# Performance work log

Measured on AMD Instinct MI355X. Metric: run time of the kernel, lower is better.

Reference implementation:

```python
import jax, jax.numpy as jnp
import numpy as np

M = 41
RHO = 4.0
HDIM = 10
NMODES = 2
BATCH = 16384


def triplet_index(m_size, rho):
    # reduced PBC triplet index set: n >= m, |m|,|n|,|m+n| <= (M-1)/2, |m*n| <= rho*(M-1)/2
    h = (m_size - 1) // 2
    idx = [(m, n) for m in range(-h, h + 1) for n in range(m, h + 1)
           if abs(m + n) <= h and abs(m * n) <= rho * h]
    return np.array(idx, dtype=np.int32)

IDX = triplet_index(M, RHO)
S = len(IDX)


def _c(a):
    # last-dim-2 real tensor -> complex
    return jax.lax.complex(a[..., 0], a[..., 1])


def setup_inputs() -> dict:
    key = jax.random.key(0)
    ks = jax.random.split(key, 6)
    x = jax.random.normal(ks[0], (BATCH, M, NMODES, 2), dtype=jnp.float32)
    task_info = jax.random.uniform(ks[1], (BATCH, 4), dtype=jnp.float32)  # col 0 = power in dBm
    pbc_C = 0.01 * jax.random.normal(ks[2], (S, 2), dtype=jnp.float32)  # complex PBC coeffs
    W1 = jax.random.normal(ks[3], (HDIM, NMODES, S, 2), dtype=jnp.float32) / np.sqrt(2.0 * NMODES * S)
    b1 = jnp.zeros((HDIM, 2), dtype=jnp.float32)
    W2 = jax.random.normal(ks[4], (HDIM, NMODES, M, 2), dtype=jnp.float32) / np.sqrt(2.0 * NMODES * M)
    b2 = jnp.zeros((HDIM, 2), dtype=jnp.float32)
    m_idx = jnp.asarray(IDX[:, 0], dtype=jnp.int32)
    n_idx = jnp.asarray(IDX[:, 1], dtype=jnp.int32)
    return {"x": x, "task_info": task_info, "pbc_C": pbc_C,
            "W1": W1, "b1": b1, "W2": W2, "b2": b2,
            "m_idx": m_idx, "n_idx": n_idx}


def _nonlinear_features(E, m_idx, n_idx):
    # E: [B, M, 2] complex -> [B, 2, S]; Manakov dual-pol triplets:
    # F[p] = (E[c+m,p]*conj(E[c+m+n,p]) + E[c+m,q]*conj(E[c+m+n,q])) * E[c+n,p]
    c = E.shape[1] // 2
    A = E[:, c + m_idx, :] * jnp.conj(E[:, c + m_idx + n_idx, :])  # [B, S, 2]
    F = (A + A[..., ::-1]) * E[:, c + n_idx, :]                    # [B, S, 2]
    return jnp.transpose(F, (0, 2, 1))                             # [B, 2, S]


def _conv_full(Wc, bc, inp):
    # ComplexConv1d whose kernel spans the whole input length (output length 1) -> [B, out]
    return jnp.einsum('oik,bik->bo', Wc, inp) + bc


def _forward(x, task_info, pbc_C, W1, b1, W2, b2, m_idx, n_idx):
    E = _c(x)                                    # [B, M, 2] complex64
    c = M // 2
    P = 10.0 ** (task_info[:, 0] / 10.0) / NMODES  # [B] launch power per mode
    F = _nonlinear_features(E, m_idx, n_idx)     # [B, 2, S]
    # EqAMPBC: center symbol + P * (triplet features . complex coeffs)
    pbc_out = E[:, c, :] + P[:, None] * jnp.einsum('bps,s->bp', F, _c(pbc_C))  # [B, 2]
    w1, bb1, w2, bb2 = _c(W1), _c(b1), _c(W2), _c(b2)
    # A = cat([f1(fo), f1(fo with pols flipped)], dim=-1) -> [B, hdim, 2]
    A = jnp.stack([_conv_full(w1, bb1, F), _conv_full(w1, bb1, F[:, ::-1, :])], axis=-1)
    Et = jnp.transpose(E, (0, 2, 1))             # [B, 2, M]
    Bm = jnp.stack([_conv_full(w2, bb2, Et), _conv_full(w2, bb2, Et[:, ::-1, :])], axis=-1)
    term = jnp.sum(A * Bm * jnp.conj(Bm) + jnp.conj(A) * Bm * Bm, axis=1)  # [B, 2]
    out = pbc_out + (1e-4 / np.sqrt(HDIM)) * term * (P[:, None] ** 2)
    return jnp.stack([out.real, out.imag], axis=-1)  # [B, 2, 2] float32


def reference(x, task_info, pbc_C, W1, b1, W2, b2, m_idx, n_idx):
    return _forward(x, task_info, pbc_C, W1, b1, W2, b2, m_idx, n_idx)
```

## Files before the change

kernel.cpp:

```cpp
#include <hip/hip_runtime.h>
#include <hip/hip_bf16.h>

typedef short bf16x8 __attribute__((ext_vector_type(8)));
typedef float f32x16 __attribute__((ext_vector_type(16)));

#define NCOL  32
#define KS1   112
#define KS2   12
#define ESTR  264

#define WP_OFF   0
#define W2P_OFF  344064

#define MET_OFF  10824
#define SUM_OFF  14544
#define LDS_BYTES 39120

__device__ __forceinline__ unsigned short f2bf(float f) {
    union { float f; unsigned u; } v; v.f = f;
    unsigned r = v.u + 0x7FFFu + ((v.u >> 16) & 1u);
    return (unsigned short)(r >> 16);
}
__device__ __forceinline__ float bfl(unsigned u) {
    union { unsigned q; float f; } v; v.q = u << 16; return v.f;
}
__device__ __forceinline__ float bfh(unsigned u) {
    union { unsigned q; float f; } v; v.q = u & 0xffff0000u; return v.f;
}
__device__ __forceinline__ unsigned pk2(float a, float b) {
    __hip_bfloat162 h = __float22bfloat162_rn(make_float2(a, b));
    unsigned u; __builtin_memcpy(&u, &h, 4); return u;
}
__device__ __forceinline__ bf16x8 asbf(uint4 v) {
    union { uint4 u; bf16x8 b; } z; z.u = v; return z.b;
}
__device__ __forceinline__ f32x16 zero16() {
    f32x16 z;
#pragma unroll
    for (int i = 0; i < 16; ++i) z[i] = 0.f;
    return z;
}

__global__ void prep_kernel(const float* __restrict__ W1,
                            const float* __restrict__ W2,
                            const float* __restrict__ pbcC,
                            unsigned short* __restrict__ Wp,
                            unsigned short* __restrict__ W2p, int S) {
    int idx = blockIdx.x * 256 + threadIdx.x;
    const int N1 = KS1 * 3 * 64 * 2;
    const int N2 = KS2 * 3 * 64 * 2;
    if (idx < N1) {
        int ks = idx / 384, rem = idx - ks * 384;
        int mt = rem >> 7; rem &= 127;
        int lane = rem >> 1, jh = rem & 1;
        int row = mt * 32 + (lane & 31);
        int kg  = ks * 16 + (lane >> 5) * 8 + jh * 4;
        int s   = kg >> 2;
        float2 wj0 = make_float2(0.f, 0.f), wj1 = make_float2(0.f, 0.f);
        int p = 0, r = 0;
        if (s < S) {
            if (row < 80) {
                int o = row >> 2; p = (row >> 1) & 1; r = row & 1;
                wj0 = ((const float2*)W1)[(size_t)(o * 2 + 0) * S + s];
                wj1 = ((const float2*)W1)[(size_t)(o * 2 + 1) * S + s];
            } else if (row < 84) {
                p = (row >> 1) & 1; r = row & 1;
                wj0 = ((const float2*)pbcC)[s];
            }
        }
        ushort4 h; unsigned short us[4];
#pragma unroll
        for (int t = 0; t < 4; ++t) {
            int i = t & 1, cc = t >> 1, j2 = i ^ p;
            float2 w = j2 ? wj1 : wj0;
            float v = (cc == 0) ? (r ? w.y : w.x) : (r ? w.x : -w.y);
            us[t] = f2bf(v);
        }
        h.x = us[0]; h.y = us[1]; h.z = us[2]; h.w = us[3];
        ((ushort4*)Wp)[idx] = h;
        return;
    }
    idx -= N1;
    if (idx < N2) {
        int ks = idx / 384, rem = idx - ks * 384;
        int mt = rem >> 7; rem &= 127;
        int lane = rem >> 1, jh = rem & 1;
        int row = mt * 32 + (lane & 31);
        int kg  = ks * 16 + (lane >> 5) * 8 + jh * 4;
        int m   = kg >> 2;
        float2 wj0 = make_float2(0.f, 0.f), wj1 = make_float2(0.f, 0.f);
        int p = 0, r = 0;
        if (m < 41 && row < 80) {
            int o = row >> 2; p = (row >> 1) & 1; r = row & 1;
            wj0 = ((const float2*)W2)[(o * 2 + 0) * 41 + m];
            wj1 = ((const float2*)W2)[(o * 2 + 1) * 41 + m];
        }
        ushort4 h; unsigned short us[4];
#pragma unroll
        for (int t = 0; t < 4; ++t) {
            int i = t & 1, cc = t >> 1, j2 = i ^ p;
            float2 w = j2 ? wj1 : wj0;
            float v = (cc == 0) ? (r ? w.y : w.x) : (r ? w.x : -w.y);
            us[t] = f2bf(v);
        }
        h.x = us[0]; h.y = us[1]; h.z = us[2]; h.w = us[3];
        ((ushort4*)W2p)[idx] = h;
    }
}

__global__ __launch_bounds__(256, 3) void eqsonn_kernel(
    const float* __restrict__ x, const float* __restrict__ task,
    const unsigned short* __restrict__ Wp,
    const unsigned short* __restrict__ W2p,
    const int* __restrict__ m_idx, const int* __restrict__ n_idx,
    const float* __restrict__ b1, const float* __restrict__ b2,
    float* __restrict__ out, int B, int S)
{
    __shared__ alignas(16) char ldsb[LDS_BYTES];
    const int tid  = threadIdx.x;
    const int lane = tid & 63;
    const int w    = __builtin_amdgcn_readfirstlane(tid >> 6);
    const int col  = lane & 31;
    const int kha  = lane >> 5;
    const int b0   = blockIdx.x * NCOL;

    for (int e = tid; e < 41 * NCOL; e += 256) {
        int bb = e / 41, k = e - bb * 41;
        int bs = b0 + bb; if (bs > B - 1) bs = B - 1;
        float4 v = ((const float4*)x)[(size_t)bs * 41 + k];
        ushort4 h;
        h.x = f2bf(v.x); h.y = f2bf(v.y); h.z = f2bf(v.z); h.w = f2bf(v.w);
        *(ushort4*)(ldsb + k * ESTR + bb * 8) = h;
    }
    for (int i = tid; i < 464; i += 256) {
        int m = 0, n = 0;
        if (i < S) { m = m_idx[i]; n = n_idx[i]; }
        unsigned offM = (unsigned)((20 + m) * ESTR);
        unsigned offB = (unsigned)((20 + m + n) * ESTR);
        unsigned offN = (unsigned)((20 + n) * ESTR);
        *(uint2*)(ldsb + MET_OFF + i * 8) = make_uint2(offM | (offB << 16), offN);
    }
    __syncthreads();

    const char* Ebase = ldsb + col * 8;
    auto ldM4 = [&](int ks) -> uint4 {
        return *(const uint4*)(ldsb + MET_OFF + (ks * 4 + kha * 2) * 8);
    };
    auto ldE = [&](unsigned off) -> uint2 {
        return *(const uint2*)(Ebase + off);
    };
    auto fbuild = [&](uint2 em, uint2 eq, uint2 en, unsigned& lo, unsigned& hi) {
        float m0r = bfl(em.x), m0i = bfh(em.x), m1r = bfl(em.y), m1i = bfh(em.y);
        float q0r = bfl(eq.x), q0i = bfh(eq.x), q1r = bfl(eq.y), q1i = bfh(eq.y);
        float n0r = bfl(en.x), n0i = bfh(en.x), n1r = bfl(en.y), n1i = bfh(en.y);
        float sr = m0r * q0r + m0i * q0i + m1r * q1r + m1i * q1i;
        float si = m0i * q0r - m0r * q0i + m1i * q1r - m1r * q1i;
        float F0r = sr * n0r - si * n0i, F0i = sr * n0i + si * n0r;
        float F1r = sr * n1r - si * n1i, F1i = sr * n1i + si * n1r;
        lo = pk2(F0r, F1r); hi = pk2(F0i, F1i);
    };

    f32x16 ac0 = zero16(), ac1 = zero16(), ac2 = zero16();
    {
        const int ks0 = w * 28;
        uint4 M = ldM4(ks0);
        uint2 e0 = ldE(M.x & 0xffffu), e1 = ldE(M.x >> 16), e2 = ldE(M.y);
        uint2 e3 = ldE(M.z & 0xffffu), e4 = ldE(M.z >> 16), e5 = ldE(M.w);
        uint4 Mc = ldM4(ks0 + 1);
        const short* Wp16 = (const short*)Wp;
        for (int ks = ks0; ks < ks0 + 28; ++ks) {
            const short* ap = Wp16 + (size_t)ks * 1536 + lane * 8;
            bf16x8 A0 = *(const bf16x8*)(ap);
            bf16x8 A1 = *(const bf16x8*)(ap + 512);
            bf16x8 A2 = *(const bf16x8*)(ap + 1024);
            uint2 f0 = ldE(Mc.x & 0xffffu), f1v = ldE(Mc.x >> 16), f2v = ldE(Mc.y);
            uint2 f3 = ldE(Mc.z & 0xffffu), f4v = ldE(Mc.z >> 16), f5v = ldE(Mc.w);
            uint4 Mn = ldM4(ks + 2);
            unsigned g0, g1, g2, g3;
            fbuild(e0, e1, e2, g0, g1);
            fbuild(e3, e4, e5, g2, g3);
            bf16x8 bfr = asbf(make_uint4(g0, g1, g2, g3));
            ac0 = __builtin_amdgcn_mfma_f32_32x32x16_bf16(A0, bfr, ac0, 0, 0, 0);
            ac1 = __builtin_amdgcn_mfma_f32_32x32x16_bf16(A1, bfr, ac1, 0, 0, 0);
            ac2 = __builtin_amdgcn_mfma_f32_32x32x16_bf16(A2, bfr, ac2, 0, 0, 0);
            e0 = f0; e1 = f1v; e2 = f2v; e3 = f3; e4 = f4v; e5 = f5v; Mc = Mn;
        }
    }

    __syncthreads();
    float* Sum = (float*)(ldsb + SUM_OFF);
    auto dump = [&](f32x16 a, int baserow, bool add) {
#pragma unroll
        for (int reg = 0; reg < 16; ++reg) {
            int row = baserow + (reg & 3) + 8 * (reg >> 2) + 4 * kha;
            int idx = row * 32 + col;
            if (add) Sum[idx] += a[reg]; else Sum[idx] = a[reg];
        }
    };
    for (int ph = 0; ph < 4; ++ph) {
        if (w == ph) {
            bool add = (ph != 0);
            dump(ac0, 0, add); dump(ac1, 32, add); dump(ac2, 64, add);
        }
        __syncthreads();
    }

    f32x16 bc0 = zero16(), bc1 = zero16(), bc2 = zero16();
    {
        const short* W216 = (const short*)W2p;
        for (int t = 0; t < 3; ++t) {
            int ks2 = w * 3 + t;
            const short* ap = W216 + (size_t)ks2 * 1536 + lane * 8;
            bf16x8 A0 = *(const bf16x8*)(ap);
            bf16x8 A1 = *(const bf16x8*)(ap + 512);
            bf16x8 A2 = *(const bf16x8*)(ap + 1024);
            unsigned g[4];
#pragma unroll
            for (int j = 0; j < 2; ++j) {
                int m = ks2 * 4 + kha * 2 + j;
                int mc = m < 41 ? m : 40;
                uint2 ue = *(const uint2*)(ldsb + mc * ESTR + col * 8);
                unsigned lo = (ue.x & 0xffffu) | (ue.y << 16);
                unsigned hi = (ue.x >> 16) | (ue.y & 0xffff0000u);
                if (m >= 41) { lo = 0u; hi = 0u; }
                g[j * 2] = lo; g[j * 2 + 1] = hi;
            }
            bf16x8 bfr = asbf(make_uint4(g[0], g[1], g[2], g[3]));
            bc0 = __builtin_amdgcn_mfma_f32_32x32x16_bf16(A0, bfr, bc0, 0, 0, 0);
            bc1 = __builtin_amdgcn_mfma_f32_32x32x16_bf16(A1, bfr, bc1, 0, 0, 0);
            bc2 = __builtin_amdgcn_mfma_f32_32x32x16_bf16(A2, bfr, bc2, 0, 0, 0);
        }
    }
    __syncthreads();
    for (int ph = 0; ph < 4; ++ph) {
        if (w == ph) {
            bool add = (ph != 0);
            dump(bc0, 96, add); dump(bc1, 128, add); dump(bc2, 160, add);
        }
        __syncthreads();
    }

    if (w == 0 && lane < NCOL) {
        int c = lane;
        float pr0 = Sum[80 * 32 + c], pi0 = Sum[81 * 32 + c];
        float pr1 = Sum[82 * 32 + c], pi1 = Sum[83 * 32 + c];
        float t0 = 0.f, t1 = 0.f, t2 = 0.f, t3 = 0.f;
#pragma unroll
        for (int o = 0; o < 10; ++o) {
            float b2r = b2[o * 2], b2i = b2[o * 2 + 1];
            float b1r = b1[o * 2], b1i = b1[o * 2 + 1];
            int rb = o * 4;
            float B0r = Sum[(96 + rb + 0) * 32 + c] + b2r;
            float B0i = Sum[(96 + rb + 1) * 32 + c] + b2i;
            float B1r = Sum[(96 + rb + 2) * 32 + c] + b2r;
            float B1i = Sum[(96 + rb + 3) * 32 + c] + b2i;
            float A0r = Sum[(rb + 0) * 32 + c] + b1r;
            float A0i = Sum[(rb + 1) * 32 + c] + b1i;
            float A1r = Sum[(rb + 2) * 32 + c] + b1r;
            float A1i = Sum[(rb + 3) * 32 + c] + b1i;
            float g0 = 2.f * (A0r * B0r + A0i * B0i);
            t0 += g0 * B0r; t1 += g0 * B0i;
            float g1 = 2.f * (A1r * B1r + A1i * B1i);
            t2 += g1 * B1r; t3 += g1 * B1i;
        }
        int b = b0 + c;
        if (b < B) {
            float dbm = task[(size_t)b * 4];
            float P   = exp2f(dbm * 0.33219280948873623f) * 0.5f;
            float kP2 = 3.1622776601683794e-05f * P * P;
            float4 Ec = ((const float4*)x)[(size_t)b * 41 + 20];
            float4 o4;
            o4.x = Ec.x + P * pr0 + kP2 * t0;
            o4.y = Ec.y + P * pi0 + kP2 * t1;
            o4.z = Ec.z + P * pr1 + kP2 * t2;
            o4.w = Ec.w + P * pi1 + kP2 * t3;
            ((float4*)out)[b] = o4;
        }
    }
}

extern "C" void kernel_launch(void* const* d_in, const int* in_sizes, int n_in,
                              void* d_out, int out_size, void* d_ws, size_t ws_size,
                              hipStream_t stream) {
    const float* x     = (const float*)d_in[0];
    const float* task  = (const float*)d_in[1];
    const float* pbcC  = (const float*)d_in[2];
    const float* W1    = (const float*)d_in[3];
    const float* b1    = (const float*)d_in[4];
    const float* W2    = (const float*)d_in[5];
    const float* b2    = (const float*)d_in[6];
    const int*   m_idx = (const int*)d_in[7];
    const int*   n_idx = (const int*)d_in[8];
    float* out = (float*)d_out;

    int S = in_sizes[7];
    int B = in_sizes[0] / (41 * 2 * 2);

    char* ws = (char*)d_ws;
    unsigned short* Wp  = (unsigned short*)(ws + WP_OFF);
    unsigned short* W2p = (unsigned short*)(ws + W2P_OFF);

    int prep_n = KS1 * 3 * 64 * 2 + KS2 * 3 * 64 * 2;
    prep_kernel<<<(prep_n + 255) / 256, 256, 0, stream>>>(W1, W2, pbcC, Wp, W2p, S);

    int grid = (B + NCOL - 1) / NCOL;
    eqsonn_kernel<<<grid, 256, 0, stream>>>(x, task, Wp, W2p, m_idx, n_idx,
                                            b1, b2, out, B, S);
}
```

Baseline: 101.7 us.

## Split K reduction across eight waves with dual LDS partial buffers and weight prefetch

Doubles the block to 512 threads so eight waves each handle 14 K-steps of the first GEMM instead of four waves handling 28. The waves reduce in two groups into two separate LDS sum buffers, which are then added together. The next step's weight fragments are also software-prefetched to hide global load latency. The cost is more LDS per block, an extra reduction pass and barriers, and a possible drop in occupancy because of the larger LDS footprint and register limits.

Result: faster. 98.08 us (-3.6%).

```diff
diff --git a/kernel.cpp b/kernel.cpp
--- a/kernel.cpp
+++ b/kernel.cpp
@@ -14,7 +14,8 @@
 
 #define MET_OFF  10824
 #define SUM_OFF  14544
-#define LDS_BYTES 39120
+#define SUM2_OFF 39120
+#define LDS_BYTES 63696
 
 __device__ __forceinline__ unsigned short f2bf(float f) {
     union { float f; unsigned u; } v; v.f = f;
@@ -108,7 +109,7 @@
     }
 }
 
-__global__ __launch_bounds__(256, 3) void eqsonn_kernel(
+__global__ __launch_bounds__(512, 4) void eqsonn_kernel(
     const float* __restrict__ x, const float* __restrict__ task,
     const unsigned short* __restrict__ Wp,
     const unsigned short* __restrict__ W2p,
@@ -124,7 +125,7 @@
     const int kha  = lane >> 5;
     const int b0   = blockIdx.x * NCOL;
 
-    for (int e = tid; e < 41 * NCOL; e += 256) {
+    for (int e = tid; e < 41 * NCOL; e += 512) {
         int bb = e / 41, k = e - bb * 41;
         int bs = b0 + bb; if (bs > B - 1) bs = B - 1;
         float4 v = ((const float4*)x)[(size_t)bs * 41 + k];
@@ -132,13 +133,13 @@
         h.x = f2bf(v.x); h.y = f2bf(v.y); h.z = f2bf(v.z); h.w = f2bf(v.w);
         *(ushort4*)(ldsb + k * ESTR + bb * 8) = h;
     }
-    for (int i = tid; i < 464; i += 256) {
+    if (tid < 464) {
         int m = 0, n = 0;
-        if (i < S) { m = m_idx[i]; n = n_idx[i]; }
+        if (tid < S) { m = m_idx[tid]; n = n_idx[tid]; }
         unsigned offM = (unsigned)((20 + m) * ESTR);
         unsigned offB = (unsigned)((20 + m + n) * ESTR);
         unsigned offN = (unsigned)((20 + n) * ESTR);
-        *(uint2*)(ldsb + MET_OFF + i * 8) = make_uint2(offM | (offB << 16), offN);
+        *(uint2*)(ldsb + MET_OFF + tid * 8) = make_uint2(offM | (offB << 16), offN);
     }
     __syncthreads();
 
@@ -162,17 +163,22 @@
 
     f32x16 ac0 = zero16(), ac1 = zero16(), ac2 = zero16();
     {
-        const int ks0 = w * 28;
+        const int ks0 = w * 14;
+        const short* Wp16 = (const short*)Wp;
         uint4 M = ldM4(ks0);
         uint2 e0 = ldE(M.x & 0xffffu), e1 = ldE(M.x >> 16), e2 = ldE(M.y);
         uint2 e3 = ldE(M.z & 0xffffu), e4 = ldE(M.z >> 16), e5 = ldE(M.w);
         uint4 Mc = ldM4(ks0 + 1);
-        const short* Wp16 = (const short*)Wp;
-        for (int ks = ks0; ks < ks0 + 28; ++ks) {
-            const short* ap = Wp16 + (size_t)ks * 1536 + lane * 8;
-            bf16x8 A0 = *(const bf16x8*)(ap);
-            bf16x8 A1 = *(const bf16x8*)(ap + 512);
-            bf16x8 A2 = *(const bf16x8*)(ap + 1024);
+        const short* ap0 = Wp16 + (size_t)ks0 * 1536 + lane * 8;
+        bf16x8 A0 = *(const bf16x8*)(ap0);
+        bf16x8 A1 = *(const bf16x8*)(ap0 + 512);
+        bf16x8 A2 = *(const bf16x8*)(ap0 + 1024);
+        for (int ks = ks0; ks < ks0 + 14; ++ks) {
+            int ksn = (ks + 1 < KS1) ? ks + 1 : KS1 - 1;
+            const short* apn = Wp16 + (size_t)ksn * 1536 + lane * 8;
+            bf16x8 N0 = *(const bf16x8*)(apn);
+            bf16x8 N1 = *(const bf16x8*)(apn + 512);
+            bf16x8 N2 = *(const bf16x8*)(apn + 1024);
             uint2 f0 = ldE(Mc.x & 0xffffu), f1v = ldE(Mc.x >> 16), f2v = ldE(Mc.y);
             uint2 f3 = ldE(Mc.z & 0xffffu), f4v = ldE(Mc.z >> 16), f5v = ldE(Mc.w);
             uint4 Mn = ldM4(ks + 2);
@@ -184,22 +190,24 @@
             ac1 = __builtin_amdgcn_mfma_f32_32x32x16_bf16(A1, bfr, ac1, 0, 0, 0);
             ac2 = __builtin_amdgcn_mfma_f32_32x32x16_bf16(A2, bfr, ac2, 0, 0, 0);
             e0 = f0; e1 = f1v; e2 = f2v; e3 = f3; e4 = f4v; e5 = f5v; Mc = Mn;
+            A0 = N0; A1 = N1; A2 = N2;
         }
     }
 
     __syncthreads();
-    float* Sum = (float*)(ldsb + SUM_OFF);
+    float* Reg = (float*)(ldsb + ((w < 4) ? SUM_OFF : SUM2_OFF));
+    const int ph = w & 3;
     auto dump = [&](f32x16 a, int baserow, bool add) {
 #pragma unroll
         for (int reg = 0; reg < 16; ++reg) {
             int row = baserow + (reg & 3) + 8 * (reg >> 2) + 4 * kha;
             int idx = row * 32 + col;
-            if (add) Sum[idx] += a[reg]; else Sum[idx] = a[reg];
+            if (add) Reg[idx] += a[reg]; else Reg[idx] = a[reg];
         }
     };
-    for (int ph = 0; ph < 4; ++ph) {
-        if (w == ph) {
-            bool add = (ph != 0);
+    for (int p = 0; p < 4; ++p) {
+        if (ph == p) {
+            bool add = (p != 0);
             dump(ac0, 0, add); dump(ac1, 32, add); dump(ac2, 64, add);
         }
         __syncthreads();
@@ -208,8 +216,7 @@
     f32x16 bc0 = zero16(), bc1 = zero16(), bc2 = zero16();
     {
         const short* W216 = (const short*)W2p;
-        for (int t = 0; t < 3; ++t) {
-            int ks2 = w * 3 + t;
+        for (int ks2 = w; ks2 < KS2; ks2 += 8) {
             const short* ap = W216 + (size_t)ks2 * 1536 + lane * 8;
             bf16x8 A0 = *(const bf16x8*)(ap);
             bf16x8 A1 = *(const bf16x8*)(ap + 512);
@@ -232,15 +239,29 @@
         }
     }
     __syncthreads();
-    for (int ph = 0; ph < 4; ++ph) {
-        if (w == ph) {
-            bool add = (ph != 0);
+    for (int p = 0; p < 4; ++p) {
+        if (ph == p) {
+            bool add = (p != 0);
             dump(bc0, 96, add); dump(bc1, 128, add); dump(bc2, 160, add);
         }
         __syncthreads();
     }
 
+    {
+        float4* S1 = (float4*)(ldsb + SUM_OFF);
+        float4* S2 = (float4*)(ldsb + SUM2_OFF);
+#pragma unroll
+        for (int i = 0; i < 3; ++i) {
+            int idx = tid + i * 512;
+            float4 a = S1[idx], b = S2[idx];
+            a.x += b.x; a.y += b.y; a.z += b.z; a.w += b.w;
+            S1[idx] = a;
+        }
+    }
+    __syncthreads();
+
     if (w == 0 && lane < NCOL) {
+        const float* Sum = (const float*)(ldsb + SUM_OFF);
         int c = lane;
         float pr0 = Sum[80 * 32 + c], pi0 = Sum[81 * 32 + c];
         float pr1 = Sum[82 * 32 + c], pi1 = Sum[83 * 32 + c];
@@ -304,6 +325,6 @@
     prep_kernel<<<(prep_n + 255) / 256, 256, 0, stream>>>(W1, W2, pbcC, Wp, W2p, S);
 
     int grid = (B + NCOL - 1) / NCOL;
-    eqsonn_kernel<<<grid, 256, 0, stream>>>(x, task, Wp, W2p, m_idx, n_idx,
+    eqsonn_kernel<<<grid, 512, 0, stream>>>(x, task, Wp, W2p, m_idx, n_idx,
                                             b1, b2, out, B, S);
 }
```
